# Kernel optimization log

Measured on AMD Instinct MI355X. Metric: run time of the kernel, lower is better.

The kernel has to match this reference:

```python
import jax, jax.numpy as jnp
import numpy as np

B, C, P, NP = 16, 768, 2048, 64
FFE = 4


def _ln(x, g, b, eps=1e-5):
    m = jnp.mean(x, axis=-1, keepdims=True)
    v = jnp.mean(jnp.square(x - m), axis=-1, keepdims=True)
    return (x - m) * jax.lax.rsqrt(v + eps) * g + b


def _gelu(x):
    return jax.nn.gelu(x, approximate=False)  # torch nn.GELU default (erf)


def _any_attn(q, k, v, nqg, nqb, nkg, nkb, nvg, nvb, wq, wk, wv, wp, bq, bk, bv, bp):
    # AnyAttention: LN each stream, project, ReLU-gated logits scaled by d^-0.5, softmax, proj
    scale = q.shape[-1] ** -0.5
    qn = _ln(q, nqg, nqb) @ wq + bq
    kn = _ln(k, nkg, nkb) @ wk + bk
    vn = _ln(v, nvg, nvb) @ wv + bv
    attn = jnp.einsum('bqc,bkc->bqk', qn, kn)
    attn = jax.nn.relu(attn) * scale  # returned attn is relu*scale (pre-softmax)
    out = jnp.einsum('bqk,bkc->bqc', jax.nn.softmax(attn, axis=-1), vn)
    return attn, out @ wp + bp


def _forward(x, parts,
             enc_nq_g, enc_nq_b, enc_nk_g, enc_nk_b, enc_nv_g, enc_nv_b,
             enc_wq, enc_wk, enc_wv, enc_wp, enc_bq, enc_bk, enc_bv, enc_bp,
             dec_nq_g, dec_nq_b, dec_nk_g, dec_nk_b, dec_nv_g, dec_nv_b,
             dec_wq, dec_wk, dec_wv, dec_wp, dec_bq, dec_bk, dec_bv, dec_bp,
             ffn_ng, ffn_nb, ffn_w1, ffn_b1, ffn_w2, ffn_b2,
             sr_w1, sr_b1, sr_w2, sr_b2):
    x = jnp.swapaxes(x, 1, 2)  # b c p -> b p c
    # SimpleReasoning: SE-style gate over part tokens (AdaptiveMaxPool1d(1) = max over channel dim)
    g = jnp.max(parts, axis=-1)                                  # [b, np]
    g = _gelu(g @ sr_w1 + sr_b1)
    gate = jax.nn.sigmoid(g @ sr_w2 + sr_b2)[..., None]          # [b, np, 1]
    parts = gate * parts + parts                                 # parts1 + parts (residual)
    # enc_attn: parts attend over image tokens
    attn0, attn_out = _any_attn(parts, x, x,
                                enc_nq_g, enc_nq_b, enc_nk_g, enc_nk_b, enc_nv_g, enc_nv_b,
                                enc_wq, enc_wk, enc_wv, enc_wp, enc_bq, enc_bk, enc_bv, enc_bp)
    attn_0 = jnp.max(attn0, axis=-1)                             # maxpool over k -> [b, np]
    parts_in = parts + attn_out
    # FFN on image tokens with residual
    h = _ln(x, ffn_ng, ffn_nb)
    feats1 = x + (_gelu(h @ ffn_w1 + ffn_b1) @ ffn_w2 + ffn_b2)
    # dec_attn: image tokens attend over part tokens
    _, feats = _any_attn(feats1, parts_in, parts_in,
                         dec_nq_g, dec_nq_b, dec_nk_g, dec_nk_b, dec_nv_g, dec_nv_b,
                         dec_wq, dec_wk, dec_wv, dec_wp, dec_bq, dec_bk, dec_bv, dec_bp)
    feats = x + feats
    return jnp.swapaxes(feats, 1, 2), attn_0                     # [b, c, p], [b, np]


def setup_inputs() -> dict:
    key = jax.random.key(0)
    ki = iter(jax.random.split(key, 48))
    def rn(shape, s=1.0):
        return jax.random.normal(next(ki), shape, jnp.float32) * s
    d = {}
    d['x'] = rn((B, C, P))
    d['parts'] = rn((B, NP, C))
    for pre in ('enc', 'dec'):
        for nm in ('nq', 'nk', 'nv'):
            d[f'{pre}_{nm}_g'] = jnp.ones((C,), jnp.float32)
            d[f'{pre}_{nm}_b'] = jnp.zeros((C,), jnp.float32)
        for nm in ('wq', 'wk', 'wv', 'wp'):
            d[f'{pre}_{nm}'] = rn((C, C), 0.02)
        for nm in ('bq', 'bk', 'bv', 'bp'):
            d[f'{pre}_{nm}'] = jnp.zeros((C,), jnp.float32)
    d['ffn_ng'] = jnp.ones((C,), jnp.float32)
    d['ffn_nb'] = jnp.zeros((C,), jnp.float32)
    d['ffn_w1'] = rn((C, FFE * C), 0.02)
    d['ffn_b1'] = jnp.zeros((FFE * C,), jnp.float32)
    d['ffn_w2'] = rn((FFE * C, C), 0.02)
    d['ffn_b2'] = jnp.zeros((C,), jnp.float32)
    d['sr_w1'] = rn((NP, NP), 0.1)
    d['sr_b1'] = jnp.zeros((NP,), jnp.float32)
    d['sr_w2'] = rn((NP, NP), 0.1)
    d['sr_b2'] = jnp.zeros((NP,), jnp.float32)
    return d


def reference(x, parts,
              enc_nq_g, enc_nq_b, enc_nk_g, enc_nk_b, enc_nv_g, enc_nv_b,
              enc_wq, enc_wk, enc_wv, enc_wp, enc_bq, enc_bk, enc_bv, enc_bp,
              dec_nq_g, dec_nq_b, dec_nk_g, dec_nk_b, dec_nv_g, dec_nv_b,
              dec_wq, dec_wk, dec_wv, dec_wp, dec_bq, dec_bk, dec_bv, dec_bp,
              ffn_ng, ffn_nb, ffn_w1, ffn_b1, ffn_w2, ffn_b2,
              sr_w1, sr_b1, sr_w2, sr_b2):
    return _forward(x, parts,
                    enc_nq_g, enc_nq_b, enc_nk_g, enc_nk_b, enc_nv_g, enc_nv_b,
                    enc_wq, enc_wk, enc_wv, enc_wp, enc_bq, enc_bk, enc_bv, enc_bp,
                    dec_nq_g, dec_nq_b, dec_nk_g, dec_nk_b, dec_nv_g, dec_nv_b,
                    dec_wq, dec_wk, dec_wv, dec_wp, dec_bq, dec_bk, dec_bv, dec_bp,
                    ffn_ng, ffn_nb, ffn_w1, ffn_b1, ffn_w2, ffn_b2,
                    sr_w1, sr_b1, sr_w2, sr_b2)
```

## Files before the change

kernel.cpp:

```cpp
#include <hip/hip_runtime.h>

typedef unsigned short u16;
typedef unsigned int u32;
typedef __bf16 bf16x8 __attribute__((ext_vector_type(8)));
typedef float f32x4 __attribute__((ext_vector_type(4)));
typedef unsigned int u32x4 __attribute__((ext_vector_type(4)));

#define BB 16
#define CC 768
#define PP 2048
#define FF 3072

__device__ __forceinline__ float b2f(u16 u) {
  unsigned int x = ((unsigned int)u) << 16;
  return __builtin_bit_cast(float, x);
}
__device__ __forceinline__ u16 f2b(float f) {
  unsigned int x = __builtin_bit_cast(unsigned int, f);
  x += 0x7fffu + ((x >> 16) & 1u);
  return (u16)(x >> 16);
}
__device__ __forceinline__ float erf_fast(float x) {
  float ax = fabsf(x);
  float t = 1.0f / fmaf(0.3275911f, ax, 1.0f);
  float p = t * fmaf(t, fmaf(t, fmaf(t, fmaf(t, 1.061405429f, -1.453152027f),
                                     1.421413741f), -0.284496736f), 0.254829592f);
  float r = 1.0f - p * __expf(-ax * ax);
  return copysignf(r, x);
}
__device__ __forceinline__ float gelu_f(float x) {
  return 0.5f * x * (1.0f + erf_fast(x * 0.7071067811865475f));
}

typedef __attribute__((address_space(1))) const unsigned int g_u32;
typedef __attribute__((address_space(3))) unsigned int l_u32;
__device__ __forceinline__ void gl_lds16(const u16* g, u16* l) {
  __builtin_amdgcn_global_load_lds((g_u32*)g, (l_u32*)l, 16, 0, 0);
}

struct Wtr10 {
  const float* W[10]; const float* g[10]; u16* O[10];
  int Kd[10]; int Nd[10]; int tr[10]; int cum[11];
};
__global__ void wtr10_k(Wtr10 a) {
  __shared__ float t[64][65];
  int tbid = blockIdx.x;
  int z = 0;
  while (tbid >= a.cum[z + 1]) ++z;
  int r = tbid - a.cum[z];
  const float* W = a.W[z];
  const float* g = a.g[z];
  u16* Wt = a.O[z];
  int K = a.Kd[z], N = a.Nd[z];
  int nbx = N >> 6;
  int n0 = (r % nbx) * 64, k0 = (r / nbx) * 64;
  int tx = threadIdx.x & 63, ty = threadIdx.x >> 6;
  if (!a.tr[z]) {
    for (int i = 0; i < 16; ++i) {
      int k = k0 + ty + i * 4;
      float sc = g ? g[k] : 1.0f;
      Wt[(long)k * N + n0 + tx] = f2b(W[(long)k * N + n0 + tx] * sc);
    }
    return;
  }
  for (int i = 0; i < 16; ++i) {
    int k = k0 + ty + i * 4;
    float sc = g ? g[k] : 1.0f;
    t[ty + i * 4][tx] = W[(long)k * N + n0 + tx] * sc;
  }
  __syncthreads();
  for (int i = 0; i < 16; ++i) {
    int n = n0 + ty + i * 4;
    Wt[(long)n * K + k0 + tx] = f2b(t[tx][ty + i * 4]);
  }
}

struct Bf7 {
  const float* b[7]; const float* nb[7]; const float* W[7]; float* o[7];
  int Kd[7]; int Nd[7];
};
__global__ void bfuse7_k(Bf7 a) {
  __shared__ float red[4][64];
  int tbid = blockIdx.x;
  int z, bx;
  if (tbid < 72) { z = tbid / 12; bx = tbid % 12; }
  else { z = 6; bx = tbid - 72; }
  const float* b = a.b[z];
  const float* nb = a.nb[z];
  const float* W = a.W[z];
  float* outb = a.o[z];
  int K = a.Kd[z], N = a.Nd[z];
  int n = bx * 64 + (threadIdx.x & 63);
  int slice = threadIdx.x >> 6;
  float acc = 0.f;
#pragma unroll 4
  for (int k = slice; k < K; k += 4) acc += nb[k] * W[(long)k * N + n];
  red[slice][threadIdx.x & 63] = acc;
  __syncthreads();
  if (slice == 0)
    outb[n] = b[n] + red[0][threadIdx.x & 63] + red[1][threadIdx.x & 63] +
              red[2][threadIdx.x & 63] + red[3][threadIdx.x & 63];
}

struct Bf2 {
  const float* b[2]; const float* nb[2]; const float* W[2]; float* o[2];
  const float* sa0; const float* sb0; float* so0;
  const float* sa1; const float* sb1; float* so1;
};
__global__ void bfuse2_k(Bf2 a) {
  if (blockIdx.x == 24) {
    if (threadIdx.x < 128) {
      int w = threadIdx.x >> 6, lane = threadIdx.x & 63;
      const float* A = w ? a.sa1 : a.sa0;
      const float* Bv = w ? a.sb1 : a.sb0;
      float s = 0.f;
      for (int i = lane; i < CC; i += 64) s += A[i] * Bv[i];
      for (int o = 32; o; o >>= 1) s += __shfl_xor(s, o);
      if (lane == 0) *(w ? a.so1 : a.so0) = s;
    }
    return;
  }
  __shared__ float red[4][64];
  int z = blockIdx.x / 12, bx = blockIdx.x % 12;
  const float* b = a.b[z];
  const float* nb = a.nb[z];
  const float* W = a.W[z];
  int n = bx * 64 + (threadIdx.x & 63);
  int slice = threadIdx.x >> 6;
  float acc = 0.f;
#pragma unroll 4
  for (int k = slice; k < CC; k += 4) acc += nb[k] * W[(long)k * CC + n];
  red[slice][threadIdx.x & 63] = acc;
  __syncthreads();
  if (slice == 0)
    a.o[z][n] = (b ? b[n] : 0.f) + red[0][threadIdx.x & 63] +
                red[1][threadIdx.x & 63] + red[2][threadIdx.x & 63] +
                red[3][threadIdx.x & 63];
}

struct Dw4 { const u16* A[4]; const float* v[4]; float* o[4]; };
__global__ void dotw4_k(Dw4 a) {
  int z = blockIdx.x / 192;
  int row = (blockIdx.x % 192) * 4 + (threadIdx.x >> 6);
  int lane = threadIdx.x & 63;
  const u16* ip = a.A[z] + (long)row * CC;
  const float* vec = a.v[z];
  float s = 0.f;
  for (int i = 0; i < 12; ++i) s += b2f(ip[lane + i * 64]) * vec[lane + i * 64];
  for (int o = 32; o; o >>= 1) s += __shfl_xor(s, o);
  if (lane == 0) a.o[z][row] = s;
}

__global__ void dotc_k(const u16* __restrict__ A, const float* __restrict__ vec,
                       const float* __restrict__ cptr, float* __restrict__ outp) {
  int row = blockIdx.x * 4 + (threadIdx.x >> 6);
  int lane = threadIdx.x & 63;
  const u16* ip = A + (long)row * CC;
  float s = 0.f;
  for (int i = 0; i < 12; ++i) s += b2f(ip[lane + i * 64]) * vec[lane + i * 64];
  for (int o = 32; o; o >>= 1) s += __shfl_xor(s, o);
  if (lane == 0) outp[row] = s + cptr[0];
}

__global__ void xprep_k(const float* __restrict__ x, float* __restrict__ mean,
                        float* __restrict__ rstd, u16* __restrict__ xh) {
  __shared__ float t[64][65];
  __shared__ float red[8][64];
  __shared__ float mn_s[64], rs_s[64];
  int p0 = blockIdx.x * 64, b = blockIdx.y;
  int tx = threadIdx.x & 63, ty = threadIdx.x >> 6;
  const float* xb = x + (long)b * CC * PP;
  float s = 0.f, sq = 0.f;
  for (int c = ty; c < CC; c += 4) {
    float f = xb[(long)c * PP + p0 + tx];
    s += f; sq += f * f;
  }
  red[ty][tx] = s;
  red[4 + ty][tx] = sq;
  __syncthreads();
  if (ty == 0) {
    float S = red[0][tx] + red[1][tx] + red[2][tx] + red[3][tx];
    float Q = red[4][tx] + red[5][tx] + red[6][tx] + red[7][tx];
    float m = S * (1.0f / 768.0f);
    float var = Q * (1.0f / 768.0f) - m * m;
    float rs = rsqrtf(var + 1e-5f);
    mn_s[tx] = m; rs_s[tx] = rs;
    int gi = (b << 11) + p0 + tx;
    mean[gi] = m; rstd[gi] = rs;
  }
  __syncthreads();
  u16* ob = xh + (long)b * PP * CC;
  for (int cb = 0; cb < 12; ++cb) {
    int c0 = cb * 64;
    for (int i = 0; i < 16; ++i)
      t[ty + i * 4][tx] = xb[(long)(c0 + ty + i * 4) * PP + p0 + tx];
    __syncthreads();
    for (int i = 0; i < 16; ++i) {
      int pl = ty + i * 4;
      ob[(long)(p0 + pl) * CC + c0 + tx] = f2b((t[tx][pl] - mn_s[pl]) * rs_s[pl]);
    }
    __syncthreads();
  }
}

__global__ void parts_gate_k(const float* __restrict__ parts,
                             const float* __restrict__ w1, const float* __restrict__ b1,
                             const float* __restrict__ w2, const float* __restrict__ b2,
                             float* __restrict__ gate_out) {
  int b = blockIdx.x, t = threadIdx.x;
  __shared__ float g[64], g1[64];
  int r = t >> 2, l4 = t & 3;
  const float* pr = parts + ((long)b * 64 + r) * CC;
  float m = -1e30f;
  for (int c = l4; c < CC; c += 4) m = fmaxf(m, pr[c]);
  m = fmaxf(m, __shfl_xor(m, 1));
  m = fmaxf(m, __shfl_xor(m, 2));
  if (l4 == 0) g[r] = m;
  __syncthreads();
  if (t < 64) {
    float a = b1[t];
    for (int k = 0; k < 64; ++k) a += g[k] * w1[k * 64 + t];
    g1[t] = gelu_f(a);
  }
  __syncthreads();
  if (t < 64) {
    float a = b2[t];
    for (int k = 0; k < 64; ++k) a += g1[k] * w2[k * 64 + t];
    gate_out[b * 64 + t] = 1.0f / (1.0f + expf(-a));
  }
}

__global__ void gate_ln_k(const float* __restrict__ parts, const float* __restrict__ gate,
                          float* __restrict__ parts1, u16* __restrict__ ph) {
  int row = blockIdx.x * 4 + (threadIdx.x >> 6);
  int lane = threadIdx.x & 63;
  float g = 1.0f + gate[row];
  const float* ip = parts + (long)row * CC;
  float* op1 = parts1 + (long)row * CC;
  float v[12];
  float s = 0.f, sq = 0.f;
  for (int i = 0; i < 12; ++i) {
    float f = ip[lane + i * 64] * g;
    v[i] = f; op1[lane + i * 64] = f;
    s += f; sq += f * f;
  }
  for (int o = 32; o; o >>= 1) { s += __shfl_xor(s, o); sq += __shfl_xor(sq, o); }
  float mean = s * (1.0f / 768.0f);
  float var = sq * (1.0f / 768.0f) - mean * mean;
  float rstd = rsqrtf(var + 1e-5f);
  u16* op = ph + (long)row * CC;
  for (int i = 0; i < 12; ++i) op[lane + i * 64] = f2b((v[i] - mean) * rstd);
}

template <typename T>
__global__ void ln_rows_k(const T* __restrict__ in, u16* __restrict__ outp, int rows) {
  int row = blockIdx.x * 4 + (threadIdx.x >> 6);
  if (row >= rows) return;
  int lane = threadIdx.x & 63;
  const T* ip = in + (long)row * CC;
  float v[12];
  float s = 0.f, sq = 0.f;
  for (int i = 0; i < 12; ++i) {
    float f;
    if constexpr (sizeof(T) == 2) f = b2f(((const u16*)ip)[lane + i * 64]);
    else f = ((const float*)ip)[lane + i * 64];
    v[i] = f; s += f; sq += f * f;
  }
  for (int o = 32; o; o >>= 1) { s += __shfl_xor(s, o); sq += __shfl_xor(sq, o); }
  float mean = s * (1.0f / 768.0f);
  float var = sq * (1.0f / 768.0f) - mean * mean;
  float rstd = rsqrtf(var + 1e-5f);
  u16* op = outp + (long)row * CC;
  for (int i = 0; i < 12; ++i) op[lane + i * 64] = f2b((v[i] - mean) * rstd);
}

__global__ void softmax_enc_k(const float* __restrict__ attn, u16* __restrict__ sm,
                              float* __restrict__ attn0) {
  int row = blockIdx.x * 4 + (threadIdx.x >> 6);
  int lane = threadIdx.x & 63;
  const float* ap = attn + (long)row * PP;
  float v[32];
  float m = -1e30f;
  for (int i = 0; i < 32; ++i) { v[i] = ap[lane + i * 64]; m = fmaxf(m, v[i]); }
  for (int o = 32; o; o >>= 1) m = fmaxf(m, __shfl_xor(m, o));
  float s = 0.f;
  for (int i = 0; i < 32; ++i) { float e = expf(v[i] - m); v[i] = e; s += e; }
  for (int o = 32; o; o >>= 1) s += __shfl_xor(s, o);
  float inv = 1.0f / s;
  u16* sp = sm + (long)row * PP;
  for (int i = 0; i < 32; ++i) sp[lane + i * 64] = f2b(v[i] * inv);
  if (lane == 0) attn0[row] = m;
}

__global__ void pvred_k(const float* __restrict__ part, u16* __restrict__ outp) {
  long i = (long)blockIdx.x * 256 + threadIdx.x;
  const f32x4* p = (const f32x4*)part;
  f32x4 a = p[i];
  a += p[i + 196608];
  a += p[i + 2 * 196608];
  a += p[i + 3 * 196608];
  u32 lo = (u32)f2b(a.x) | ((u32)f2b(a.y) << 16);
  u32 hi = (u32)f2b(a.z) | ((u32)f2b(a.w) << 16);
  ((u32*)outp)[i * 2] = lo;
  ((u32*)outp)[i * 2 + 1] = hi;
}

template <int EPI>
__global__ __launch_bounds__(256) void gemmf_k(
    const u16* __restrict__ A, const u16* __restrict__ Bm, void* __restrict__ Cm,
    const float* __restrict__ bias, int M, int N, int K, int lda,
    const float* __restrict__ res32) {
  __shared__ __align__(16) u16 As[128 * 32];
  __shared__ __align__(16) u16 Bs[128 * 32];
  const int nbx = N >> 7;
  const int nwg = gridDim.x;
  int tile = blockIdx.x;
  if ((nwg & 7) == 0) {
    tile = (tile & 7) * (nwg >> 3) + (tile >> 3);
  }
  const int bm0 = (tile / nbx) << 7;
  const int bn0 = (tile % nbx) << 7;
  const int tid = threadIdx.x;
  const int lane = tid & 63;
  const int wave = tid >> 6;
  const int laneq = lane & 15, lanek = lane >> 4;
  const int wm = (wave >> 1) << 6, wn = (wave & 1) << 6;
  const int srow = wave * 32 + (lane >> 2);
  const int scol = (lane & 3) << 3;
  const u16* Ag0 = A + (long)(bm0 + srow) * lda + scol;
  const u16* Ag1 = A + (long)(bm0 + srow + 16) * lda + scol;
  const u16* Bg0 = Bm + (long)(bn0 + srow) * K + scol;
  const u16* Bg1 = Bm + (long)(bn0 + srow + 16) * K + scol;
  u16* lA0 = As + wave * 1024;
  u16* lA1 = As + wave * 1024 + 512;
  u16* lB0 = Bs + wave * 1024;
  u16* lB1 = Bs + wave * 1024 + 512;
  f32x4 acc[4][4] = {};
  for (int k0 = 0; k0 < K; k0 += 32) {
    gl_lds16(Ag0 + k0, lA0);
    gl_lds16(Ag1 + k0, lA1);
    gl_lds16(Bg0 + k0, lB0);
    gl_lds16(Bg1 + k0, lB1);
    __syncthreads();
    bf16x8 af[4], bfr[4];
#pragma unroll
    for (int i = 0; i < 4; ++i)
      af[i] = *(const bf16x8*)(As + (wm + i * 16 + laneq) * 32 + (lanek << 3));
#pragma unroll
    for (int i = 0; i < 4; ++i)
      bfr[i] = *(const bf16x8*)(Bs + (wn + i * 16 + laneq) * 32 + (lanek << 3));
#pragma unroll
    for (int mi = 0; mi < 4; ++mi)
#pragma unroll
      for (int ni = 0; ni < 4; ++ni)
        acc[mi][ni] =
            __builtin_amdgcn_mfma_f32_16x16x32_bf16(af[mi], bfr[ni], acc[mi][ni], 0, 0, 0);
    __syncthreads();
  }
#pragma unroll
  for (int mi = 0; mi < 4; ++mi) {
#pragma unroll
    for (int r = 0; r < 4; ++r) {
      const int row = bm0 + wm + mi * 16 + (lanek << 2) + r;
#pragma unroll
      for (int ni = 0; ni < 4; ++ni) {
        const int col = bn0 + wn + ni * 16 + laneq;
        float v = acc[mi][ni][r] + (bias ? bias[col] : 0.f);
        long off = (long)row * N + col;
        if constexpr (EPI == 0) {
          ((u16*)Cm)[off] = f2b(v);
        } else {
          ((float*)Cm)[off] = v + res32[off];
        }
      }
    }
  }
}

struct G4 { const u16* A[4]; const u16* B[4]; u16* C[4]; };
__global__ __launch_bounds__(256) void gemmf4_k(G4 a) {
  __shared__ __align__(16) u16 As[128 * 32];
  __shared__ __align__(16) u16 Bs[128 * 32];
  const int z = blockIdx.x / 36;
  const int r = blockIdx.x % 36;
  const u16* A = a.A[z];
  const u16* Bm = a.B[z];
  u16* Cm = a.C[z];
  const int bm0 = (r / 6) << 7;
  const int bn0 = (r % 6) << 7;
  const int tid = threadIdx.x;
  const int lane = tid & 63;
  const int wave = tid >> 6;
  const int laneq = lane & 15, lanek = lane >> 4;
  const int wm = (wave >> 1) << 6, wn = (wave & 1) << 6;
  const int srow = wave * 32 + (lane >> 2);
  const int scol = (lane & 3) << 3;
  const u16* Ag0 = A + (long)(bm0 + srow) * CC + scol;
  const u16* Ag1 = A + (long)(bm0 + srow + 16) * CC + scol;
  const u16* Bg0 = Bm + (long)(bn0 + srow) * CC + scol;
  const u16* Bg1 = Bm + (long)(bn0 + srow + 16) * CC + scol;
  u16* lA0 = As + wave * 1024;
  u16* lA1 = As + wave * 1024 + 512;
  u16* lB0 = Bs + wave * 1024;
  u16* lB1 = Bs + wave * 1024 + 512;
  f32x4 acc[4][4] = {};
  for (int k0 = 0; k0 < CC; k0 += 32) {
    gl_lds16(Ag0 + k0, lA0);
    gl_lds16(Ag1 + k0, lA1);
    gl_lds16(Bg0 + k0, lB0);
    gl_lds16(Bg1 + k0, lB1);
    __syncthreads();
    bf16x8 af[4], bfr[4];
#pragma unroll
    for (int i = 0; i < 4; ++i)
      af[i] = *(const bf16x8*)(As + (wm + i * 16 + laneq) * 32 + (lanek << 3));
#pragma unroll
    for (int i = 0; i < 4; ++i)
      bfr[i] = *(const bf16x8*)(Bs + (wn + i * 16 + laneq) * 32 + (lanek << 3));
#pragma unroll
    for (int mi = 0; mi < 4; ++mi)
#pragma unroll
      for (int ni = 0; ni < 4; ++ni)
        acc[mi][ni] =
            __builtin_amdgcn_mfma_f32_16x16x32_bf16(af[mi], bfr[ni], acc[mi][ni], 0, 0, 0);
    __syncthreads();
  }
#pragma unroll
  for (int mi = 0; mi < 4; ++mi)
#pragma unroll
    for (int r2 = 0; r2 < 4; ++r2) {
      const int row = bm0 + wm + mi * 16 + (lanek << 2) + r2;
#pragma unroll
      for (int ni = 0; ni < 4; ++ni) {
        const int col = bn0 + wn + ni * 16 + laneq;
        Cm[(long)row * CC + col] = f2b(acc[mi][ni][r2]);
      }
    }
}

#define G256_BAR() __builtin_amdgcn_s_barrier()
#define G256_WLGKM0()                                    \
  do {                                                   \
    asm volatile("s_waitcnt lgkmcnt(0)" ::: "memory");   \
    __builtin_amdgcn_sched_barrier(0);                   \
  } while (0)
#define G256_RD_A(HALF)                                                        \
  _Pragma("unroll") for (int m2 = 0; m2 < 4; ++m2) {                           \
    af[m2 * 2 + 0] = *(const bf16x8*)(Ab + ar + (HALF)*4096 + m2 * 1024 + g0); \
    af[m2 * 2 + 1] = *(const bf16x8*)(Ab + ar + (HALF)*4096 + m2 * 1024 + g1); \
  }
#define G256_RD_B(HALF, BFR)                                                   \
  _Pragma("unroll") for (int n2 = 0; n2 < 2; ++n2) {                           \
    BFR[n2 * 2 + 0] = *(const bf16x8*)(Bb + br + (HALF)*2048 + n2 * 1024 + g0);\
    BFR[n2 * 2 + 1] = *(const bf16x8*)(Bb + br + (HALF)*2048 + n2 * 1024 + g1);\
  }
#define G256_MFMA_Q(H, NH, BFR)                                                \
  __builtin_amdgcn_s_setprio(1);                                               \
  _Pragma("unroll") for (int m2 = 0; m2 < 4; ++m2)                             \
  _Pragma("unroll") for (int n2 = 0; n2 < 2; ++n2)                             \
  _Pragma("unroll") for (int s = 0; s < 2; ++s)                                \
      acc[(H)*4 + m2][(NH)*2 + n2] = __builtin_amdgcn_mfma_f32_16x16x32_bf16(  \
          af[m2 * 2 + s], BFR[n2 * 2 + s], acc[(H)*4 + m2][(NH)*2 + n2], 0, 0, 0); \
  __builtin_amdgcn_s_setprio(0);

template <int EPI>
__device__ __forceinline__ void g256_body(
    u16* As, u16* Bs, int tileIn, int nwg,
    const u16* __restrict__ A, const u16* __restrict__ Bm, void* __restrict__ Cm,
    const float* __restrict__ bias, int M, int N, int K,
    const u16* __restrict__ rxh, const float* __restrict__ rmean,
    const float* __restrict__ rrstd, long rro) {
  const int nbx = N >> 8;
  int tile = tileIn;
  if ((nwg & 7) == 0) {
    tile = (tile & 7) * (nwg >> 3) + (tile >> 3);
  }
  const int bm0 = (tile / nbx) << 8;
  const int bn0 = (tile % nbx) << 8;
  const int tid = threadIdx.x;
  const int lane = tid & 63;
  const int wave = tid >> 6;
  const int laneq = lane & 15, lanek = lane >> 4;
  const int wrow = (wave >> 2) << 7;
  const int wcol = (wave & 3) << 6;
  const int srow8 = lane >> 3;
  const int sg = (lane & 7) ^ srow8;
  const u16* gA = A + (long)(bm0 + wave * 8 + srow8) * K + sg * 8;
  const u16* gB = Bm + (long)(bn0 + wave * 8 + srow8) * K + sg * 8;
  const long lineK = (long)64 * K;
  const int ldsLine = wave * 512;
  const int gx = laneq & 7;
  const int g0 = ((lanek) ^ gx) << 3;
  const int g1 = ((lanek + 4) ^ gx) << 3;
  const int ar = (wrow + laneq) * 64;
  const int br = (wcol + laneq) * 64;
  f32x4 acc[8][4] = {};
  bf16x8 af[8], bfr0[4], bfr1[4];
  const int NT = K >> 6;

  {
    u16* dA = As;
    u16* dB = Bs;
    gl_lds16(gA, dA + ldsLine);
    gl_lds16(gA + lineK, dA + ldsLine + 4096);
    gl_lds16(gA + 2 * lineK, dA + ldsLine + 8192);
    gl_lds16(gA + 3 * lineK, dA + ldsLine + 12288);
    gl_lds16(gB, dB + ldsLine);
    gl_lds16(gB + lineK, dB + ldsLine + 4096);
    gl_lds16(gB + 2 * lineK, dB + ldsLine + 8192);
    gl_lds16(gB + 3 * lineK, dB + ldsLine + 12288);
  }
  for (int T = 0; T < NT; ++T) {
    const u16* Ab = As + (T & 1) * 16384;
    const u16* Bb = Bs + (T & 1) * 16384;
    u16* An = As + ((T & 1) ^ 1) * 16384;
    u16* Bn = Bs + ((T & 1) ^ 1) * 16384;
    const long ko = (long)(T + 1) * 64;
    const bool more = (T + 1 < NT);
    if (more) {
      gl_lds16(gA + ko, An + ldsLine);
      gl_lds16(gA + ko + lineK, An + ldsLine + 4096);
      gl_lds16(gB + ko, Bn + ldsLine);
      gl_lds16(gB + ko + lineK, Bn + ldsLine + 4096);
      asm volatile("s_waitcnt vmcnt(4)" ::: "memory");
    } else {
      asm volatile("s_waitcnt vmcnt(0)" ::: "memory");
    }
    G256_BAR();
    G256_RD_A(0);
    G256_RD_B(0, bfr0);
    G256_WLGKM0();
    G256_MFMA_Q(0, 0, bfr0);
    G256_BAR();
    if (more) {
      gl_lds16(gA + ko + 2 * lineK, An + ldsLine + 8192);
      gl_lds16(gA + ko + 3 * lineK, An + ldsLine + 12288);
      gl_lds16(gB + ko + 2 * lineK, Bn + ldsLine + 8192);
      gl_lds16(gB + ko + 3 * lineK, Bn + ldsLine + 12288);
    }
    G256_RD_B(1, bfr1);
    G256_BAR();
    G256_WLGKM0();
    G256_MFMA_Q(0, 1, bfr1);
    G256_BAR();
    G256_RD_A(1);
    G256_BAR();
    G256_WLGKM0();
    G256_MFMA_Q(1, 1, bfr1);
    G256_BAR();
    G256_MFMA_Q(1, 0, bfr0);
  }

#pragma unroll
  for (int mi = 0; mi < 8; ++mi) {
#pragma unroll
    for (int r = 0; r < 4; ++r) {
      const int row = bm0 + wrow + mi * 16 + (lanek << 2) + r;
      float mn = 0.f, istd = 0.f;
      if constexpr (EPI == 3) {
        long gr = rro + row;
        mn = rmean[gr];
        istd = 1.0f / rrstd[gr];
      }
#pragma unroll
      for (int ni = 0; ni < 4; ++ni) {
        const int col = bn0 + wcol + ni * 16 + laneq;
        float v = acc[mi][ni][r] + bias[col];
        long off = (long)row * N + col;
        if constexpr (EPI == 0) {
          ((u16*)Cm)[off] = f2b(v);
        } else if constexpr (EPI == 1) {
          ((u16*)Cm)[off] = f2b(gelu_f(v));
        } else {
          v += b2f(rxh[(rro + row) * 768 + col]) * istd + mn;
          ((u16*)Cm)[off] = f2b(v);
        }
      }
    }
  }
}

template <int EPI>
__global__ __launch_bounds__(512, 2) void gemm256_k(
    const u16* __restrict__ A, const u16* __restrict__ Bm, void* __restrict__ Cm,
    const float* __restrict__ bias, int M, int N, int K,
    const u16* __restrict__ rxh, const float* __restrict__ rmean,
    const float* __restrict__ rrstd, long rro) {
  __shared__ __align__(16) u16 As[2 * 16384];
  __shared__ __align__(16) u16 Bs[2 * 16384];
  g256_body<EPI>(As, Bs, blockIdx.x, gridDim.x, A, Bm, Cm, bias, M, N, K,
                 rxh, rmean, rrstd, rro);
}

__global__ __launch_bounds__(512, 2) void ffn_mix_k(
    const u16* __restrict__ ff1a, const u16* __restrict__ W2T,
    u16* __restrict__ outDn, const float* __restrict__ b2,
    const u16* __restrict__ xh2, const u16* __restrict__ W1T,
    u16* __restrict__ ff1b, const float* __restrict__ b1f,
    const u16* __restrict__ rxh, const float* __restrict__ rmean,
    const float* __restrict__ rrstd) {
  __shared__ __align__(16) u16 As[2 * 16384];
  __shared__ __align__(16) u16 Bs[2 * 16384];
  if ((int)blockIdx.x < 192) {
    g256_body<3>(As, Bs, blockIdx.x, 192, ff1a, W2T, outDn, b2,
                 16384, CC, FF, rxh, rmean, rrstd, 0);
  } else {
    g256_body<1>(As, Bs, blockIdx.x - 192, 768, xh2, W1T, ff1b, b1f,
                 16384, FF, CC, nullptr, nullptr, nullptr, 0);
  }
}

template <int EPI, bool BNT, int TM, int TN>
__global__ __launch_bounds__(256) void gemm_k(
    const u16* __restrict__ A, const u16* __restrict__ Bm, void* __restrict__ Cm,
    const float* __restrict__ bias, int M, int N, int kLen, int lda, int ldB,
    long sA, long sB, long sC, float scale, const float* __restrict__ res32,
    const float* __restrict__ radd) {
  __shared__ __align__(16) u16 As[TM][40];
  __shared__ __align__(16) u16 Bs[TN][40];
  const int bn0 = blockIdx.x * TN;
  const int bm0 = (EPI == 4) ? 0 : blockIdx.y * TM;
  const int kOff = (EPI == 4) ? blockIdx.y * kLen : 0;
  const int bz = blockIdx.z;
  const u16* Ab = A + (long)bz * sA;
  const u16* Bb = Bm + (long)bz * sB;
  const long coff = (EPI == 4) ? ((long)blockIdx.y * gridDim.z + bz) * sC
                               : (long)bz * sC;
  const int tid = threadIdx.x;
  const int lane = tid & 63;
  const int wave = tid >> 6;
  const int wm = (TM == 64) ? 0 : ((TN == 64) ? wave * 32 : ((wave >> 1) << 6));
  const int wn = (TN == 64) ? 0 : ((TM == 64) ? wave * 32 : ((wave & 1) << 6));
  constexpr int MI = (TN == 64) ? 2 : 4;
  constexpr int NI = (TM == 64) ? 2 : 4;
  const int laneq = lane & 15, lanek = lane >> 4;
  f32x4 acc[MI][NI] = {};
  for (int k0 = 0; k0 < kLen; k0 += 32) {
    __syncthreads();
#pragma unroll
    for (int j = 0; j < TM / 64; ++j) {
      int v = tid + j * 256;
      int m = v >> 2, kcl = (v & 3) << 3;
      u32x4 val = {0, 0, 0, 0};
      if (bm0 + m < M)
        val = *(const u32x4*)(Ab + (long)(bm0 + m) * lda + kOff + k0 + kcl);
      *(u32x4*)(&As[m][kcl]) = val;
    }
    if constexpr (BNT) {
#pragma unroll
      for (int j = 0; j < TN / 64; ++j) {
        int v = tid + j * 256;
        int n = v >> 2, kcl = (v & 3) << 3;
        u32x4 val = {0, 0, 0, 0};
        if (bn0 + n < N)
          val = *(const u32x4*)(Bb + (long)(bn0 + n) * ldB + kOff + k0 + kcl);
        *(u32x4*)(&Bs[n][kcl]) = val;
      }
    } else {
      constexpr int CCH = TN / 8;
#pragma unroll
      for (int j = 0; j < TN / 64; ++j) {
        int v = tid + j * 256;
        int kk = v / CCH, nc = (v % CCH) << 3;
        u32x4 val = {0, 0, 0, 0};
        if (bn0 + nc < N)
          val = *(const u32x4*)(Bb + (long)(kOff + k0 + kk) * ldB + bn0 + nc);
        union { u32x4 v4; u16 u[8]; } uu;
        uu.v4 = val;
#pragma unroll
        for (int e = 0; e < 8; ++e) Bs[nc + e][kk] = uu.u[e];
      }
    }
    __syncthreads();
    bf16x8 af[MI], bfr[NI];
#pragma unroll
    for (int i = 0; i < MI; ++i)
      af[i] = *(const bf16x8*)(&As[wm + i * 16 + laneq][lanek << 3]);
#pragma unroll
    for (int i = 0; i < NI; ++i)
      bfr[i] = *(const bf16x8*)(&Bs[wn + i * 16 + laneq][lanek << 3]);
#pragma unroll
    for (int mi = 0; mi < MI; ++mi)
#pragma unroll
      for (int ni = 0; ni < NI; ++ni)
        acc[mi][ni] =
            __builtin_amdgcn_mfma_f32_16x16x32_bf16(af[mi], bfr[ni], acc[mi][ni], 0, 0, 0);
  }
#pragma unroll
  for (int mi = 0; mi < MI; ++mi) {
#pragma unroll
    for (int ni = 0; ni < NI; ++ni) {
      int col = bn0 + wn + ni * 16 + laneq;
      if (col >= N) continue;
#pragma unroll
      for (int r = 0; r < 4; ++r) {
        int row = bm0 + wm + mi * 16 + (lanek << 2) + r;
        if (row >= M) continue;
        float v = acc[mi][ni][r];
        long off = coff + (long)row * N + col;
        if constexpr (EPI == 2) {
          v += radd ? radd[(long)bz * M + row] : 0.f;
          ((float*)Cm)[off] = fmaxf(v, 0.0f) * scale;
        } else {
          ((float*)Cm)[off] = v;
        }
      }
    }
  }
}

__global__ __launch_bounds__(256) void decattn_k(
    const u16* __restrict__ fh, const u16* __restrict__ GVW,
    const float* __restrict__ kdotv, const float* __restrict__ x,
    const float* __restrict__ bias, float* __restrict__ outp, float scale) {
  __shared__ __align__(16) u16 As[128][40];
  __shared__ __align__(16) u16 Bs[64][40];
  __shared__ __align__(16) u16 Vs[768][68];
  __shared__ __align__(16) u16 Ps[128][72];
  __shared__ float Ts[4][1024];
  const int bm0 = blockIdx.x * 128;
  const int bz = blockIdx.y;
  const int tid = threadIdx.x, lane = tid & 63, wave = tid >> 6;
  const int laneq = lane & 15, lanek = lane >> 4;
  {
    const u16* vw = GVW + ((long)bz * 64) * 1536 + 768;
    for (int it = 0; it < 24; ++it) {
      int l8 = tid + it * 256;
      int j = l8 / 96;
      int c8 = (l8 % 96) * 8;
      union { bf16x8 v; u16 u[8]; } uu;
      uu.v = *(const bf16x8*)(vw + (long)j * 1536 + c8);
#pragma unroll
      for (int e = 0; e < 8; ++e) Vs[c8 + e][j] = uu.u[e];
    }
  }
  const u16* Ab = fh + (long)bz * PP * CC;
  const u16* Bb = GVW + (long)bz * 64 * 1536;
  const int wm = wave * 32;
  f32x4 acc[2][4] = {};
  for (int k0 = 0; k0 < CC; k0 += 32) {
    __syncthreads();
#pragma unroll
    for (int j = 0; j < 2; ++j) {
      int v = tid + j * 256;
      int m = v >> 2, kcl = (v & 3) << 3;
      *(u32x4*)(&As[m][kcl]) =
          *(const u32x4*)(Ab + (long)(bm0 + m) * CC + k0 + kcl);
    }
    {
      int n = tid >> 2, kcl = (tid & 3) << 3;
      *(u32x4*)(&Bs[n][kcl]) = *(const u32x4*)(Bb + (long)n * 1536 + k0 + kcl);
    }
    __syncthreads();
    bf16x8 af[2], bfr[4];
#pragma unroll
    for (int i = 0; i < 2; ++i)
      af[i] = *(const bf16x8*)(&As[wm + i * 16 + laneq][lanek << 3]);
#pragma unroll
    for (int i = 0; i < 4; ++i)
      bfr[i] = *(const bf16x8*)(&Bs[i * 16 + laneq][lanek << 3]);
#pragma unroll
    for (int mi = 0; mi < 2; ++mi)
#pragma unroll
      for (int ni = 0; ni < 4; ++ni)
        acc[mi][ni] =
            __builtin_amdgcn_mfma_f32_16x16x32_bf16(af[mi], bfr[ni], acc[mi][ni], 0, 0, 0);
  }
#pragma unroll
  for (int mi = 0; mi < 2; ++mi) {
#pragma unroll
    for (int r = 0; r < 4; ++r) {
      float e[4];
      float mx = -1e30f;
#pragma unroll
      for (int ni = 0; ni < 4; ++ni) {
        const int col = ni * 16 + laneq;
        float v = acc[mi][ni][r] + kdotv[(long)bz * 64 + col];
        v = fmaxf(v, 0.0f) * scale;
        e[ni] = v;
        mx = fmaxf(mx, v);
      }
      mx = fmaxf(mx, __shfl_xor(mx, 1));
      mx = fmaxf(mx, __shfl_xor(mx, 2));
      mx = fmaxf(mx, __shfl_xor(mx, 4));
      mx = fmaxf(mx, __shfl_xor(mx, 8));
      float s = 0.f;
#pragma unroll
      for (int ni = 0; ni < 4; ++ni) { e[ni] = __expf(e[ni] - mx); s += e[ni]; }
      s += __shfl_xor(s, 1);
      s += __shfl_xor(s, 2);
      s += __shfl_xor(s, 4);
      s += __shfl_xor(s, 8);
      float inv = 1.0f / s;
      const int prow = wm + mi * 16 + (lanek << 2) + r;
#pragma unroll
      for (int ni = 0; ni < 4; ++ni)
        Ps[prow][ni * 16 + laneq] = f2b(e[ni] * inv);
    }
  }
  __syncthreads();
  const int wr = (wave & 1) << 6;
  const int wc = (wave >> 1) << 6;
  const long obase = (long)bz * CC * PP;
  const int pbase = bm0 + wr + (lane & 3) * 16;
  for (int nc = 0; nc < 6; ++nc) {
    f32x4 a2[4][4] = {};
#pragma unroll
    for (int ks = 0; ks < 2; ++ks) {
      bf16x8 af[4], bfr[4];
#pragma unroll
      for (int i = 0; i < 4; ++i)
        af[i] = *(const bf16x8*)(&Ps[wr + i * 16 + laneq][ks * 32 + (lanek << 3)]);
#pragma unroll
      for (int i = 0; i < 4; ++i)
        bfr[i] = *(const bf16x8*)(&Vs[nc * 128 + wc + i * 16 + laneq]
                                     [ks * 32 + (lanek << 3)]);
#pragma unroll
      for (int mi = 0; mi < 4; ++mi)
#pragma unroll
        for (int ni = 0; ni < 4; ++ni)
          a2[mi][ni] =
              __builtin_amdgcn_mfma_f32_16x16x32_bf16(af[mi], bfr[ni], a2[mi][ni], 0, 0, 0);
    }
    float* smem = Ts[wave];
#pragma unroll
    for (int ni = 0; ni < 4; ++ni) {
#pragma unroll
      for (int mi = 0; mi < 4; ++mi)
#pragma unroll
        for (int r = 0; r < 4; ++r) {
          const int col = nc * 128 + wc + ni * 16 + laneq;
          smem[(mi * 16 + (lanek << 2) + r) * 16 + laneq] =
              a2[mi][ni][r] + bias[col];
        }
      const int c = nc * 128 + wc + ni * 16 + (lane >> 2);
      const float* xs = x + obase + (long)c * PP + pbase;
      float* os = outp + obase + (long)c * PP + pbase;
      const float* sr = smem + (lane & 3) * 256 + (lane >> 2);
#pragma unroll
      for (int q4 = 0; q4 < 4; ++q4) {
        f32x4 xv = *(const f32x4*)(xs + q4 * 4);
        f32x4 ov;
        ov.x = sr[(q4 * 4 + 0) * 16] + xv.x;
        ov.y = sr[(q4 * 4 + 1) * 16] + xv.y;
        ov.z = sr[(q4 * 4 + 2) * 16] + xv.z;
        ov.w = sr[(q4 * 4 + 3) * 16] + xv.w;
        *(f32x4*)(os + q4 * 4) = ov;
      }
    }
  }
}

extern "C" void kernel_launch(void* const* d_in, const int* in_sizes, int n_in,
                              void* d_out, int out_size, void* d_ws, size_t ws_size,
                              hipStream_t stream) {
  (void)in_sizes; (void)n_in; (void)out_size;
  const float* x        = (const float*)d_in[0];
  const float* parts    = (const float*)d_in[1];
  const float* enc_nq_g = (const float*)d_in[2];
  const float* enc_nq_b = (const float*)d_in[3];
  const float* enc_nk_g = (const float*)d_in[4];
  const float* enc_nk_b = (const float*)d_in[5];
  const float* enc_nv_g = (const float*)d_in[6];
  const float* enc_nv_b = (const float*)d_in[7];
  const float* enc_wq   = (const float*)d_in[8];
  const float* enc_wk   = (const float*)d_in[9];
  const float* enc_wv   = (const float*)d_in[10];
  const float* enc_wp   = (const float*)d_in[11];
  const float* enc_bq   = (const float*)d_in[12];
  const float* enc_bk   = (const float*)d_in[13];
  const float* enc_bv   = (const float*)d_in[14];
  const float* enc_bp   = (const float*)d_in[15];
  const float* dec_nq_g = (const float*)d_in[16];
  const float* dec_nq_b = (const float*)d_in[17];
  const float* dec_nk_g = (const float*)d_in[18];
  const float* dec_nk_b = (const float*)d_in[19];
  const float* dec_nv_g = (const float*)d_in[20];
  const float* dec_nv_b = (const float*)d_in[21];
  const float* dec_wq   = (const float*)d_in[22];
  const float* dec_wk   = (const float*)d_in[23];
  const float* dec_wv   = (const float*)d_in[24];
  const float* dec_wp   = (const float*)d_in[25];
  const float* dec_bq   = (const float*)d_in[26];
  const float* dec_bk   = (const float*)d_in[27];
  const float* dec_bv   = (const float*)d_in[28];
  const float* dec_bp   = (const float*)d_in[29];
  const float* ffn_ng   = (const float*)d_in[30];
  const float* ffn_nb   = (const float*)d_in[31];
  const float* ffn_w1   = (const float*)d_in[32];
  const float* ffn_b1   = (const float*)d_in[33];
  const float* ffn_w2   = (const float*)d_in[34];
  const float* ffn_b2   = (const float*)d_in[35];
  const float* sr_w1    = (const float*)d_in[36];
  const float* sr_b1    = (const float*)d_in[37];
  const float* sr_w2    = (const float*)d_in[38];
  const float* sr_b2    = (const float*)d_in[39];
  float* outp = (float*)d_out;

  char* base = (char*)d_ws;
  size_t used = 0;
  auto alloc = [&](size_t bytes) -> void* {
    void* p = base + used;
    used += (bytes + 255) & ~(size_t)255;
    return p;
  };
  const long MC = (long)CC * CC;
  u16* WpeT = (u16*)alloc(MC * 2);
  u16* WpdT = (u16*)alloc(MC * 2);
  u16* W1T  = (u16*)alloc((long)CC * FF * 2);
  u16* W2T  = (u16*)alloc((long)CC * FF * 2);
  u16* WkR  = (u16*)alloc(MC * 2);
  u16* WqR  = (u16*)alloc(MC * 2);
  u16* WvS  = (u16*)alloc(MC * 2);
  u16* WqdR = (u16*)alloc(MC * 2);
  u16* WkdR = (u16*)alloc(MC * 2);
  u16* WvdR = (u16*)alloc(MC * 2);
  u16* m2w  = (u16*)alloc(MC * 2);
  u16* Bqk  = (u16*)alloc(MC * 2);
  u16* Bgv  = (u16*)alloc(MC * 2 * 2);
  float* bqe  = (float*)alloc(CC * 4);
  float* bke  = (float*)alloc(CC * 4);
  float* bve  = (float*)alloc(CC * 4);
  float* bqd  = (float*)alloc(CC * 4);
  float* bkd  = (float*)alloc(CC * 4);
  float* bvd  = (float*)alloc(CC * 4);
  float* b1f  = (float*)alloc(FF * 4);
  float* bias2   = (float*)alloc(CC * 4);
  float* bias_gv = (float*)alloc(2 * CC * 4);
  float* bq2     = (float*)alloc(CC * 4);
  float* wqb     = (float*)alloc(CC * 4);
  float* wkb     = (float*)alloc(CC * 4);
  float* cq      = (float*)alloc(256);
  float* ck      = (float*)alloc(256);
  float* meanx = (float*)alloc((long)BB * PP * 4);
  float* rstdx = (float*)alloc((long)BB * PP * 4);
  const long BPC = (long)BB * PP * CC;
  u16* bufA = (u16*)alloc(BPC * 2);
  u16* bufB = (u16*)alloc(BPC * 2);
  const long PC = (long)BB * 64 * CC;
  float* parts1   = (float*)alloc(PC * 4);
  float* gateb    = (float*)alloc((long)BB * 64 * 4);
  u16*   p1hat    = (u16*)alloc(PC * 2);
  u16*   qtil     = (u16*)alloc(PC * 2);
  float* qdotv    = (float*)alloc((long)BB * 64 * 4);
  float* attn_e   = (float*)alloc((long)BB * 64 * PP * 4);
  u16*   sm_e     = (u16*)alloc((long)BB * 64 * PP * 2);
  u16*   pv_e     = (u16*)alloc(PC * 2);
  float* pvpart   = (float*)alloc((long)4 * PC * 4);
  float* parts_in = (float*)alloc(PC * 4);
  u16*   pin_hat  = (u16*)alloc(PC * 2);
  u16*   GVW      = (u16*)alloc(PC * 2 * 2);
  float* kdotv    = (float*)alloc((long)BB * 64 * 4);
  int chunk_rows = 16384;
  while (chunk_rows > 4096 &&
         used + (size_t)chunk_rows * FF * 2 > ws_size)
    chunk_rows >>= 1;
  u16* ff1a = (u16*)alloc((long)chunk_rows * FF * 2);
  bool dual = (chunk_rows == 16384) &&
              (used + (size_t)chunk_rows * FF * 2 <= ws_size);
  u16* ff1b = nullptr;
  if (dual) ff1b = (u16*)alloc((long)chunk_rows * FF * 2);
  if (used > ws_size) return;

  const float scale = 0.03608439182435161f;
  dim3 blk(256);
  dim3 blk2(512);

  {
    Wtr10 wa;
    const float* Ws[10] = {enc_wp, dec_wp, ffn_w1, ffn_w2, enc_wk,
                           enc_wq, enc_wv, dec_wq, dec_wk, dec_wv};
    const float* gs[10] = {nullptr, nullptr, ffn_ng, nullptr, enc_nk_g,
                           enc_nq_g, enc_nv_g, dec_nq_g, dec_nk_g, dec_nv_g};
    u16* Os[10] = {WpeT, WpdT, W1T, W2T, WkR, WqR, WvS, WqdR, WkdR, WvdR};
    int Ks[10] = {CC, CC, CC, FF, CC, CC, CC, CC, CC, CC};
    int Ns[10] = {CC, CC, FF, CC, CC, CC, CC, CC, CC, CC};
    int tr[10] = {1, 1, 1, 1, 0, 0, 0, 0, 0, 0};
    int cum = 0;
    for (int i = 0; i < 10; ++i) {
      wa.W[i] = Ws[i]; wa.g[i] = gs[i]; wa.O[i] = Os[i];
      wa.Kd[i] = Ks[i]; wa.Nd[i] = Ns[i]; wa.tr[i] = tr[i];
      wa.cum[i] = cum;
      cum += (Ns[i] / 64) * (Ks[i] / 64);
    }
    wa.cum[10] = cum;
    wtr10_k<<<cum, blk, 0, stream>>>(wa);
    Bf7 ba;
    const float* bs[7] = {enc_bq, enc_bk, enc_bv, dec_bq, dec_bk, dec_bv, ffn_b1};
    const float* nbs[7] = {enc_nq_b, enc_nk_b, enc_nv_b, dec_nq_b, dec_nk_b,
                           dec_nv_b, ffn_nb};
    const float* ws[7] = {enc_wq, enc_wk, enc_wv, dec_wq, dec_wk, dec_wv, ffn_w1};
    float* os[7] = {bqe, bke, bve, bqd, bkd, bvd, b1f};
    for (int i = 0; i < 7; ++i) {
      ba.b[i] = bs[i]; ba.nb[i] = nbs[i]; ba.W[i] = ws[i]; ba.o[i] = os[i];
      ba.Kd[i] = CC; ba.Nd[i] = (i == 6) ? FF : CC;
    }
    bfuse7_k<<<120, blk, 0, stream>>>(ba);
    Bf2 b2a;
    b2a.b[0] = enc_bp;  b2a.nb[0] = bve; b2a.W[0] = enc_wp; b2a.o[0] = bias2;
    b2a.b[1] = nullptr; b2a.nb[1] = bvd; b2a.W[1] = dec_wp; b2a.o[1] = bias_gv + CC;
    b2a.sa0 = bqe; b2a.sb0 = bke; b2a.so0 = cq;
    b2a.sa1 = bkd; b2a.sb1 = bqd; b2a.so1 = ck;
    bfuse2_k<<<25, blk, 0, stream>>>(b2a);
    Dw4 da;
    da.A[0] = WkR;  da.v[0] = bqe; da.o[0] = bq2;
    da.A[1] = WqR;  da.v[1] = bke; da.o[1] = wqb;
    da.A[2] = WqdR; da.v[2] = bkd; da.o[2] = bias_gv;
    da.A[3] = WkdR; da.v[3] = bqd; da.o[3] = wkb;
    dotw4_k<<<768, blk, 0, stream>>>(da);
    G4 ga;
    ga.A[0] = WpeT; ga.B[0] = WvS;  ga.C[0] = m2w;
    ga.A[1] = WkR;  ga.B[1] = WqR;  ga.C[1] = Bqk;
    ga.A[2] = WqdR; ga.B[2] = WkdR; ga.C[2] = Bgv;
    ga.A[3] = WpdT; ga.B[3] = WvdR; ga.C[3] = Bgv + MC;
    gemmf4_k<<<144, blk, 0, stream>>>(ga);
  }

  xprep_k<<<dim3(32, 16), blk, 0, stream>>>(x, meanx, rstdx, bufA);

  parts_gate_k<<<16, blk, 0, stream>>>(parts, sr_w1, sr_b1, sr_w2, sr_b2, gateb);
  gate_ln_k<<<256, blk, 0, stream>>>(parts, gateb, parts1, p1hat);

  gemmf_k<0><<<48, blk, 0, stream>>>(p1hat, Bqk, qtil, bq2, 1024, CC, CC, CC,
      nullptr);
  dotc_k<<<256, blk, 0, stream>>>(p1hat, wqb, cq, qdotv);

  gemm_k<2, true, 64, 128><<<dim3(16, 1, 16), blk, 0, stream>>>(
      qtil, bufA, attn_e, nullptr, 64, PP, CC, CC, CC,
      (long)64 * CC, (long)PP * CC, (long)64 * PP, scale, nullptr, qdotv);
  softmax_enc_k<<<256, blk, 0, stream>>>(attn_e, sm_e, outp + (long)BB * CC * PP);
  gemm_k<4, false, 64, 128><<<dim3(6, 4, 16), blk, 0, stream>>>(
      sm_e, bufA, pvpart, nullptr, 64, CC, PP / 4, PP, CC,
      (long)64 * PP, (long)PP * CC, (long)64 * CC, 0.f, nullptr, nullptr);
  pvred_k<<<768, blk, 0, stream>>>(pvpart, pv_e);
  gemmf_k<4><<<48, blk, 0, stream>>>(pv_e, m2w, parts_in, bias2, 1024, CC, CC, CC,
      parts1);

  ln_rows_k<float><<<256, blk, 0, stream>>>(parts_in, pin_hat, 1024);
  gemmf_k<0><<<96, blk, 0, stream>>>(pin_hat, Bgv, GVW, bias_gv, 1024, 2 * CC, CC,
      CC, nullptr);
  dotc_k<<<256, blk, 0, stream>>>(pin_hat, wkb, ck, kdotv);

  if (dual) {
    gemm256_k<1><<<768, blk2, 0, stream>>>(bufA, W1T, ff1a, b1f, 16384, FF, CC,
        nullptr, nullptr, nullptr, 0);
    ffn_mix_k<<<960, blk2, 0, stream>>>(ff1a, W2T, bufB, ffn_b2,
        bufA + (long)16384 * CC, W1T, ff1b, b1f, bufA, meanx, rstdx);
    gemm256_k<3><<<192, blk2, 0, stream>>>(ff1b, W2T, bufB + (long)16384 * CC,
        ffn_b2, 16384, CC, FF, bufA, meanx, rstdx, 16384);
  } else {
    for (long r0 = 0; r0 < 32768; r0 += chunk_rows) {
      gemm256_k<1><<<(chunk_rows / 256) * 12, blk2, 0, stream>>>(
          bufA + r0 * CC, W1T, ff1a, b1f, chunk_rows, FF, CC,
          nullptr, nullptr, nullptr, 0);
      gemm256_k<3><<<(chunk_rows / 256) * 3, blk2, 0, stream>>>(
          ff1a, W2T, bufB + r0 * CC, ffn_b2, chunk_rows, CC, FF,
          bufA, meanx, rstdx, r0);
    }
  }
  ln_rows_k<u16><<<8192, blk, 0, stream>>>(bufB, bufB, 32768);

  decattn_k<<<dim3(16, 16), blk, 0, stream>>>(
      bufB, GVW, kdotv, x, dec_bp, outp, scale);
}
```

Measured before the change: 1.005 ms.

## Overlap FFN row LayerNorm with down-proj GEMM and decoder attention via co-scheduled kernels

Splits the standalone LayerNorm over FFN output rows into two halves and runs each half inside spare blocks of another kernel. The first half runs alongside the second down-projection GEMM, and the second half runs alongside decoder attention on the first 8 batches. The remaining 8 batches of decoder attention then run in a separate launch. The goal is to hide the memory-bound LN pass behind compute-bound work and drop one full-grid launch, at the cost of an extra decattn launch and possible contention for compute units.

```diff
diff --git a/kernel.cpp b/kernel.cpp
--- a/kernel.cpp
+++ b/kernel.cpp
@@ -250,6 +250,22 @@
   float rstd = rsqrtf(var + 1e-5f);
   u16* op = ph + (long)row * CC;
   for (int i = 0; i < 12; ++i) op[lane + i * 64] = f2b((v[i] - mean) * rstd);
+}
+
+__device__ __forceinline__ void ln_row_u16(u16* __restrict__ buf, int row) {
+  int lane = threadIdx.x & 63;
+  u16* ip = buf + (long)row * CC;
+  float v[12];
+  float s = 0.f, sq = 0.f;
+  for (int i = 0; i < 12; ++i) {
+    float f = b2f(ip[lane + i * 64]);
+    v[i] = f; s += f; sq += f * f;
+  }
+  for (int o = 32; o; o >>= 1) { s += __shfl_xor(s, o); sq += __shfl_xor(sq, o); }
+  float mean = s * (1.0f / 768.0f);
+  float var = sq * (1.0f / 768.0f) - mean * mean;
+  float rstd = rsqrtf(var + 1e-5f);
+  for (int i = 0; i < 12; ++i) ip[lane + i * 64] = f2b((v[i] - mean) * rstd);
 }
 
 template <typename T>
@@ -610,6 +626,23 @@
   }
 }
 
+__global__ __launch_bounds__(512, 2) void dn_ln_k(
+    const u16* __restrict__ ff1b, const u16* __restrict__ W2T,
+    u16* __restrict__ outDn, const float* __restrict__ b2,
+    const u16* __restrict__ rxh, const float* __restrict__ rmean,
+    const float* __restrict__ rrstd, u16* __restrict__ lnbuf) {
+  __shared__ __align__(16) u16 As[2 * 16384];
+  __shared__ __align__(16) u16 Bs[2 * 16384];
+  if ((int)blockIdx.x < 192) {
+    g256_body<3>(As, Bs, blockIdx.x, 192, ff1b, W2T, outDn, b2,
+                 16384, CC, FF, rxh, rmean, rrstd, 16384);
+  } else {
+    int w = threadIdx.x >> 6;
+    for (int r = ((int)blockIdx.x - 192) * 8 + w; r < 16384; r += 64 * 8)
+      ln_row_u16(lnbuf, r);
+  }
+}
+
 template <int EPI, bool BNT, int TM, int TN>
 __global__ __launch_bounds__(256) void gemm_k(
     const u16* __restrict__ A, const u16* __restrict__ Bm, void* __restrict__ Cm,
@@ -709,17 +742,19 @@
   }
 }
 
-__global__ __launch_bounds__(256) void decattn_k(
+struct DecSmem {
+  u16 As[128][40];
+  u16 Bs[64][40];
+  u16 Vs[768][68];
+  u16 Ps[128][72];
+  float Ts[4][1024];
+};
+
+__device__ __forceinline__ void decattn_body(
+    DecSmem& S, int bm0, int bz,
     const u16* __restrict__ fh, const u16* __restrict__ GVW,
     const float* __restrict__ kdotv, const float* __restrict__ x,
     const float* __restrict__ bias, float* __restrict__ outp, float scale) {
-  __shared__ __align__(16) u16 As[128][40];
-  __shared__ __align__(16) u16 Bs[64][40];
-  __shared__ __align__(16) u16 Vs[768][68];
-  __shared__ __align__(16) u16 Ps[128][72];
-  __shared__ float Ts[4][1024];
-  const int bm0 = blockIdx.x * 128;
-  const int bz = blockIdx.y;
   const int tid = threadIdx.x, lane = tid & 63, wave = tid >> 6;
   const int laneq = lane & 15, lanek = lane >> 4;
   {
@@ -731,7 +766,7 @@
       union { bf16x8 v; u16 u[8]; } uu;
       uu.v = *(const bf16x8*)(vw + (long)j * 1536 + c8);
 #pragma unroll
-      for (int e = 0; e < 8; ++e) Vs[c8 + e][j] = uu.u[e];
+      for (int e = 0; e < 8; ++e) S.Vs[c8 + e][j] = uu.u[e];
     }
   }
   const u16* Ab = fh + (long)bz * PP * CC;
@@ -744,21 +779,21 @@
     for (int j = 0; j < 2; ++j) {
       int v = tid + j * 256;
       int m = v >> 2, kcl = (v & 3) << 3;
-      *(u32x4*)(&As[m][kcl]) =
+      *(u32x4*)(&S.As[m][kcl]) =
           *(const u32x4*)(Ab + (long)(bm0 + m) * CC + k0 + kcl);
     }
     {
       int n = tid >> 2, kcl = (tid & 3) << 3;
-      *(u32x4*)(&Bs[n][kcl]) = *(const u32x4*)(Bb + (long)n * 1536 + k0 + kcl);
+      *(u32x4*)(&S.Bs[n][kcl]) = *(const u32x4*)(Bb + (long)n * 1536 + k0 + kcl);
     }
     __syncthreads();
     bf16x8 af[2], bfr[4];
 #pragma unroll
     for (int i = 0; i < 2; ++i)
-      af[i] = *(const bf16x8*)(&As[wm + i * 16 + laneq][lanek << 3]);
+      af[i] = *(const bf16x8*)(&S.As[wm + i * 16 + laneq][lanek << 3]);
 #pragma unroll
     for (int i = 0; i < 4; ++i)
-      bfr[i] = *(const bf16x8*)(&Bs[i * 16 + laneq][lanek << 3]);
+      bfr[i] = *(const bf16x8*)(&S.Bs[i * 16 + laneq][lanek << 3]);
 #pragma unroll
     for (int mi = 0; mi < 2; ++mi)
 #pragma unroll
@@ -795,7 +830,7 @@
       const int prow = wm + mi * 16 + (lanek << 2) + r;
 #pragma unroll
       for (int ni = 0; ni < 4; ++ni)
-        Ps[prow][ni * 16 + laneq] = f2b(e[ni] * inv);
+        S.Ps[prow][ni * 16 + laneq] = f2b(e[ni] * inv);
     }
   }
   __syncthreads();
@@ -810,11 +845,11 @@
       bf16x8 af[4], bfr[4];
 #pragma unroll
       for (int i = 0; i < 4; ++i)
-        af[i] = *(const bf16x8*)(&Ps[wr + i * 16 + laneq][ks * 32 + (lanek << 3)]);
+        af[i] = *(const bf16x8*)(&S.Ps[wr + i * 16 + laneq][ks * 32 + (lanek << 3)]);
 #pragma unroll
       for (int i = 0; i < 4; ++i)
-        bfr[i] = *(const bf16x8*)(&Vs[nc * 128 + wc + i * 16 + laneq]
-                                     [ks * 32 + (lanek << 3)]);
+        bfr[i] = *(const bf16x8*)(&S.Vs[nc * 128 + wc + i * 16 + laneq]
+                                      [ks * 32 + (lanek << 3)]);
 #pragma unroll
       for (int mi = 0; mi < 4; ++mi)
 #pragma unroll
@@ -822,7 +857,7 @@
           a2[mi][ni] =
               __builtin_amdgcn_mfma_f32_16x16x32_bf16(af[mi], bfr[ni], a2[mi][ni], 0, 0, 0);
     }
-    float* smem = Ts[wave];
+    float* smem = S.Ts[wave];
 #pragma unroll
     for (int ni = 0; ni < 4; ++ni) {
 #pragma unroll
@@ -848,6 +883,33 @@
         *(f32x4*)(os + q4 * 4) = ov;
       }
     }
+  }
+}
+
+__global__ __launch_bounds__(256) void decattn_k(
+    const u16* __restrict__ fh, const u16* __restrict__ GVW,
+    const float* __restrict__ kdotv, const float* __restrict__ x,
+    const float* __restrict__ bias, float* __restrict__ outp, float scale,
+    int bzOff) {
+  __shared__ DecSmem S;
+  decattn_body(S, blockIdx.x * 128, blockIdx.y + bzOff, fh, GVW, kdotv, x,
+               bias, outp, scale);
+}
+
+__global__ __launch_bounds__(256) void da_ln_k(
+    const u16* __restrict__ fh, const u16* __restrict__ GVW,
+    const float* __restrict__ kdotv, const float* __restrict__ x,
+    const float* __restrict__ bias, float* __restrict__ outp, float scale,
+    u16* __restrict__ lnbuf) {
+  __shared__ DecSmem S;
+  if ((int)blockIdx.x < 128) {
+    decattn_body(S, (blockIdx.x & 15) * 128, blockIdx.x >> 4, fh, GVW, kdotv,
+                 x, bias, outp, scale);
+  } else {
+    int w = threadIdx.x >> 6;
+    for (int r = 16384 + ((int)blockIdx.x - 128) * 4 + w; r < 32768;
+         r += 128 * 4)
+      ln_row_u16(lnbuf, r);
   }
 }
 
@@ -1046,8 +1108,12 @@
         nullptr, nullptr, nullptr, 0);
     ffn_mix_k<<<960, blk2, 0, stream>>>(ff1a, W2T, bufB, ffn_b2,
         bufA + (long)16384 * CC, W1T, ff1b, b1f, bufA, meanx, rstdx);
-    gemm256_k<3><<<192, blk2, 0, stream>>>(ff1b, W2T, bufB + (long)16384 * CC,
-        ffn_b2, 16384, CC, FF, bufA, meanx, rstdx, 16384);
+    dn_ln_k<<<256, blk2, 0, stream>>>(ff1b, W2T, bufB + (long)16384 * CC,
+        ffn_b2, bufA, meanx, rstdx, bufB);
+    da_ln_k<<<256, blk, 0, stream>>>(bufB, GVW, kdotv, x, dec_bp, outp, scale,
+        bufB);
+    decattn_k<<<dim3(16, 8), blk, 0, stream>>>(bufB, GVW, kdotv, x, dec_bp,
+        outp, scale, 8);
   } else {
     for (long r0 = 0; r0 < 32768; r0 += chunk_rows) {
       gemm256_k<1><<<(chunk_rows / 256) * 12, blk2, 0, stream>>>(
@@ -1057,9 +1123,8 @@
           ff1a, W2T, bufB + r0 * CC, ffn_b2, chunk_rows, CC, FF,
           bufA, meanx, rstdx, r0);
     }
-  }
-  ln_rows_k<u16><<<8192, blk, 0, stream>>>(bufB, bufB, 32768);
-
-  decattn_k<<<dim3(16, 16), blk, 0, stream>>>(
-      bufB, GVW, kdotv, x, dec_bp, outp, scale);
-}
+    ln_rows_k<u16><<<8192, blk, 0, stream>>>(bufB, bufB, 32768);
+    decattn_k<<<dim3(16, 16), blk, 0, stream>>>(bufB, GVW, kdotv, x, dec_bp,
+        outp, scale, 0);
+  }
+}
```

Result: slower. 1.070 ms (+6.5%).
